# Optimization experiments

Hardware: AMD Instinct MI355X
Metric: run time of the kernel (lower is better)

Reference implementation:

```python
import jax, jax.numpy as jnp
import numpy as np

B, S, D, H, DH, DF = 8, 1024, 512, 8, 64, 2048
EPS = 1e-5


def layer_norm(x, g, b):
    mu = jnp.mean(x, axis=-1, keepdims=True)
    var = jnp.mean(jnp.square(x - mu), axis=-1, keepdims=True)
    return (x - mu) * jax.lax.rsqrt(var + EPS) * g + b


def rel_shift(x):
    # Transformer-XL relative shift: [b,h,q,k] -> shifted [b,h,q,k]
    b, h, q, k = x.shape
    x = jnp.pad(x, ((0, 0), (0, 0), (0, 0), (1, 0)))
    x = x.reshape(b, h, k + 1, q)[:, :, 1:, :].reshape(b, h, q, k)
    return x


def setup_inputs() -> dict:
    key = jax.random.key(0)
    ks = jax.random.split(key, 16)
    sc = 0.02
    inp = {
        'x': jax.random.normal(ks[0], (B, S, D), jnp.float32),
        'rel_positions': jax.random.normal(ks[1], (S, D), jnp.float32),
        'mask': jnp.triu(jnp.ones((S, S), jnp.bool_), k=1),  # True = masked (causal)
        'Wq': jax.random.normal(ks[2], (D, D), jnp.float32) * sc,
        'Wk': jax.random.normal(ks[3], (D, D), jnp.float32) * sc,
        'Wv': jax.random.normal(ks[4], (D, D), jnp.float32) * sc,
        'Wr': jax.random.normal(ks[5], (D, D), jnp.float32) * sc,
        'Wo': jax.random.normal(ks[6], (D, D), jnp.float32) * sc,
        'u_bias': jax.random.normal(ks[7], (H, DH), jnp.float32) * sc,
        'v_bias': jax.random.normal(ks[8], (H, DH), jnp.float32) * sc,
        'ln1_g': jnp.ones((D,), jnp.float32),
        'ln1_b': jnp.zeros((D,), jnp.float32),
        'W1': jax.random.normal(ks[9], (D, DF), jnp.float32) * sc,
        'b1': jnp.zeros((DF,), jnp.float32),
        'W2': jax.random.normal(ks[10], (DF, D), jnp.float32) * sc,
        'b2': jnp.zeros((D,), jnp.float32),
        'ln2_g': jnp.ones((D,), jnp.float32),
        'ln2_b': jnp.zeros((D,), jnp.float32),
    }
    return inp


def reference(x, rel_positions, mask, Wq, Wk, Wv, Wr, Wo, u_bias, v_bias,
              ln1_g, ln1_b, W1, b1, W2, b2, ln2_g, ln2_b):
    b, s, d = x.shape
    q = (x @ Wq).reshape(b, s, H, DH)
    k = (x @ Wk).reshape(b, s, H, DH)
    v = (x @ Wv).reshape(b, s, H, DH)
    r = (rel_positions @ Wr).reshape(s, H, DH)
    # content term (q + u) k^T and position term (q + v) r^T with rel-shift
    ac = jnp.einsum('bqhd,bkhd->bhqk', q + u_bias, k)
    bd = rel_shift(jnp.einsum('bqhd,khd->bhqk', q + v_bias, r))
    scores = (ac + bd) * (1.0 / np.sqrt(DH))
    scores = jnp.where(mask[None, None, :, :], jnp.asarray(-1e9, scores.dtype), scores)
    attn = jax.nn.softmax(scores, axis=-1)
    ctx = jnp.einsum('bhqk,bkhd->bqhd', attn, v).reshape(b, s, d) @ Wo
    h1 = layer_norm(x + ctx, ln1_g, ln1_b)
    ff = jax.nn.relu(h1 @ W1 + b1) @ W2 + b2
    out = layer_norm(h1 + ff, ln2_g, ln2_b)
    return out, attn
```

## Files before the change

### kernel.cpp

```cpp
#include <hip/hip_runtime.h>
#include <hip/hip_bf16.h>

typedef __hip_bfloat16 bf16;

#define NB 8
#define NS 1024
#define ND 512
#define NH 8
#define NDH 64
#define NDF 2048

typedef __attribute__((ext_vector_type(8))) short s16x8;
typedef __attribute__((ext_vector_type(4))) float f32x4;

__device__ __forceinline__ void storev(float* p, float v) { *p = v; }
__device__ __forceinline__ void storev(bf16* p, float v) { *p = __float2bfloat16(v); }
__device__ __forceinline__ short f2bf(float f) {
    bf16 h = __float2bfloat16(f);
    return *reinterpret_cast<short*>(&h);
}
__device__ __forceinline__ float bf2f(short s) {
    bf16 h = *reinterpret_cast<bf16*>(&s);
    return __bfloat162float(h);
}

__device__ __forceinline__ void gload_lds16(const short* g, short* l) {
    __builtin_amdgcn_global_load_lds(
        (const __attribute__((address_space(1))) unsigned int*)g,
        (__attribute__((address_space(3))) unsigned int*)l, 16, 0, 0);
}

__global__ __launch_bounds__(256) void cast2_kernel(
    const float4* __restrict__ inA, int n4a,
    const float4* __restrict__ inB, int n4b,
    short* __restrict__ outA, short* __restrict__ outB)
{
    int i = blockIdx.x * 256 + threadIdx.x;
    const float4* s; short* d; int j;
    if (i < n4a) { s = inA; d = outA; j = i; }
    else if (i < n4a + n4b) { s = inB; d = outB; j = i - n4a; }
    else return;
    float4 v = s[j];
    short4 o;
    o.x = f2bf(v.x); o.y = f2bf(v.y); o.z = f2bf(v.z); o.w = f2bf(v.w);
    *reinterpret_cast<short4*>(d + (size_t)j * 4) = o;
}

struct TP7 {
    const float* src[7];
    short* dst[7];
    int K[7];
    int N[7];
};

__global__ __launch_bounds__(256) void transpose_cast_all_kernel(TP7 p)
{
    __shared__ float t[32][33];
    const int z = blockIdx.z;
    const float* src = p.src[z];
    short* dst = p.dst[z];
    const int K = p.K[z], N = p.N[z];
    const int ntx = N >> 5;
    const int f = blockIdx.x;
    if (f >= ntx * (K >> 5)) return;
    const int n0 = (f % ntx) * 32, k0 = (f / ntx) * 32;
    const int tx = threadIdx.x & 31, ty = threadIdx.x >> 5;
#pragma unroll
    for (int i = 0; i < 4; ++i)
        t[ty + i * 8][tx] = src[(size_t)(k0 + ty + i * 8) * N + n0 + tx];
    __syncthreads();
#pragma unroll
    for (int i = 0; i < 4; ++i)
        dst[(size_t)(n0 + ty + i * 8) * K + k0 + tx] = f2bf(t[tx][ty + i * 8]);
}

__global__ __launch_bounds__(256) void transpose_v_kernel(
    const short* __restrict__ v, short* __restrict__ vT)
{
    __shared__ short t[32][33];
    const int s0 = blockIdx.x * 32, n0 = blockIdx.y * 32;
    const int bh = blockIdx.z;
    const int h = bh & (NH - 1), b = bh >> 3;
    const int tx = threadIdx.x & 31, ty = threadIdx.x >> 5;
#pragma unroll
    for (int i = 0; i < 4; ++i)
        t[ty + i * 8][tx] = v[(size_t)(b * NS + s0 + ty + i * 8) * ND + h * NDH + n0 + tx];
    __syncthreads();
#pragma unroll
    for (int i = 0; i < 4; ++i)
        vT[((size_t)bh * NDH + n0 + ty + i * 8) * NS + s0 + tx] = t[tx][ty + i * 8];
}

template <typename CT>
__global__ __launch_bounds__(256) void mfma_gemm_kernel(
    const short* __restrict__ A, const short* __restrict__ Bt,
    const float* __restrict__ bias, CT* __restrict__ C,
    int M, int N, int K, int doRelu)
{
    __shared__ __align__(16) short As[128 * 32];
    __shared__ __align__(16) short Bs[128 * 32];
    const int row0 = blockIdx.y * 128;
    const int col0 = blockIdx.x * 128;
    const int tid = threadIdx.x;
    const int lane = tid & 63, w = tid >> 6;
    const int wm = w >> 1, wn = w & 1;
    const int lm = lane & 15, kq = lane >> 4;
    const int srow = lane >> 2;
    const int schk = lane & 3;

    f32x4 acc[4][4] = {};

    for (int k0 = 0; k0 < K; k0 += 32) {
#pragma unroll
        for (int p = 0; p < 2; ++p) {
            int rbase = p * 64 + w * 16;
            int r = rbase + srow;
            int gc = schk ^ ((r >> 1) & 3);
            gload_lds16(A  + (size_t)(row0 + r) * K + k0 + gc * 8, As + rbase * 32);
            gload_lds16(Bt + (size_t)(col0 + r) * K + k0 + gc * 8, Bs + rbase * 32);
        }
        __syncthreads();

        s16x8 af[4], bfr[4];
#pragma unroll
        for (int i = 0; i < 4; ++i) {
            int ra = wm * 64 + i * 16 + lm;
            int rb = wn * 64 + i * 16 + lm;
            af[i]  = *reinterpret_cast<const s16x8*>(As + ra * 32 + (kq ^ ((ra >> 1) & 3)) * 8);
            bfr[i] = *reinterpret_cast<const s16x8*>(Bs + rb * 32 + (kq ^ ((rb >> 1) & 3)) * 8);
        }
#pragma unroll
        for (int i = 0; i < 4; ++i)
#pragma unroll
            for (int j = 0; j < 4; ++j)
                acc[i][j] = __builtin_amdgcn_mfma_f32_16x16x32_bf16(
                    af[i], bfr[j], acc[i][j], 0, 0, 0);
        __syncthreads();
    }

#pragma unroll
    for (int i = 0; i < 4; ++i) {
        int cr0 = row0 + wm * 64 + i * 16 + kq * 4;
#pragma unroll
        for (int j = 0; j < 4; ++j) {
            int cc = col0 + wn * 64 + j * 16 + lm;
            float bv = bias ? bias[cc] : 0.0f;
#pragma unroll
            for (int r = 0; r < 4; ++r) {
                float v = acc[i][j][r] + bv;
                if (doRelu) v = fmaxf(v, 0.0f);
                storev(&C[(size_t)(cr0 + r) * N + cc], v);
            }
        }
    }
}

template <typename CT>
__global__ __launch_bounds__(256) void mfma_gemm64_kernel(
    const short* __restrict__ A, const short* __restrict__ Bt,
    const float* __restrict__ bias, CT* __restrict__ C,
    int M, int N, int K, int doRelu)
{
    __shared__ __align__(16) short As[128 * 32];
    __shared__ __align__(16) short Bs[64 * 32];
    const int row0 = blockIdx.y * 128;
    const int col0 = blockIdx.x * 64;
    const int tid = threadIdx.x;
    const int lane = tid & 63, w = tid >> 6;
    const int wm = w >> 1, wn = w & 1;
    const int lm = lane & 15, kq = lane >> 4;
    const int srow = lane >> 2;
    const int schk = lane & 3;

    f32x4 acc[4][2] = {};

    for (int k0 = 0; k0 < K; k0 += 32) {
#pragma unroll
        for (int p = 0; p < 2; ++p) {
            int rbase = p * 64 + w * 16;
            int r = rbase + srow;
            int gc = schk ^ ((r >> 1) & 3);
            gload_lds16(A + (size_t)(row0 + r) * K + k0 + gc * 8, As + rbase * 32);
        }
        {
            int rbase = w * 16;
            int r = rbase + srow;
            int gc = schk ^ ((r >> 1) & 3);
            gload_lds16(Bt + (size_t)(col0 + r) * K + k0 + gc * 8, Bs + rbase * 32);
        }
        __syncthreads();

        s16x8 af[4], bfr[2];
#pragma unroll
        for (int i = 0; i < 4; ++i) {
            int ra = wm * 64 + i * 16 + lm;
            af[i] = *reinterpret_cast<const s16x8*>(As + ra * 32 + (kq ^ ((ra >> 1) & 3)) * 8);
        }
#pragma unroll
        for (int j = 0; j < 2; ++j) {
            int rb = wn * 32 + j * 16 + lm;
            bfr[j] = *reinterpret_cast<const s16x8*>(Bs + rb * 32 + (kq ^ ((rb >> 1) & 3)) * 8);
        }
#pragma unroll
        for (int i = 0; i < 4; ++i)
#pragma unroll
            for (int j = 0; j < 2; ++j)
                acc[i][j] = __builtin_amdgcn_mfma_f32_16x16x32_bf16(
                    af[i], bfr[j], acc[i][j], 0, 0, 0);
        __syncthreads();
    }

#pragma unroll
    for (int i = 0; i < 4; ++i) {
        int cr0 = row0 + wm * 64 + i * 16 + kq * 4;
#pragma unroll
        for (int j = 0; j < 2; ++j) {
            int cc = col0 + wn * 32 + j * 16 + lm;
            float bv = bias ? bias[cc] : 0.0f;
#pragma unroll
            for (int r = 0; r < 4; ++r) {
                float v = acc[i][j][r] + bv;
                if (doRelu) v = fmaxf(v, 0.0f);
                storev(&C[(size_t)(cr0 + r) * N + cc], v);
            }
        }
    }
}

__global__ __launch_bounds__(256) void qkvr_gemm_kernel(
    const short* __restrict__ x_bf, const short* __restrict__ Wqkv,
    const short* __restrict__ rel_bf, const short* __restrict__ WrT,
    const float* __restrict__ ub, const float* __restrict__ vb,
    short* __restrict__ qu, short* __restrict__ qv,
    short* __restrict__ kb, short* __restrict__ vbuf,
    short* __restrict__ r_bf)
{
    const int isRel = blockIdx.x >= 12;
    if (isRel && blockIdx.y >= 8) return;
    const short* A  = isRel ? rel_bf : x_bf;
    const short* Bt = isRel ? WrT : Wqkv;
    const int col0 = isRel ? (blockIdx.x - 12) * 128 : blockIdx.x * 128;
    const int row0 = blockIdx.y * 128;

    __shared__ __align__(16) short As[128 * 32];
    __shared__ __align__(16) short Bs[128 * 32];
    const int tid = threadIdx.x;
    const int lane = tid & 63, w = tid >> 6;
    const int wm = w >> 1, wn = w & 1;
    const int lm = lane & 15, kq = lane >> 4;
    const int srow = lane >> 2;
    const int schk = lane & 3;

    f32x4 acc[4][4] = {};

    for (int k0 = 0; k0 < ND; k0 += 32) {
#pragma unroll
        for (int p = 0; p < 2; ++p) {
            int rbase = p * 64 + w * 16;
            int r = rbase + srow;
            int gc = schk ^ ((r >> 1) & 3);
            gload_lds16(A  + (size_t)(row0 + r) * ND + k0 + gc * 8, As + rbase * 32);
            gload_lds16(Bt + (size_t)(col0 + r) * ND + k0 + gc * 8, Bs + rbase * 32);
        }
        __syncthreads();

        s16x8 af[4], bfr[4];
#pragma unroll
        for (int i = 0; i < 4; ++i) {
            int ra = wm * 64 + i * 16 + lm;
            int rb = wn * 64 + i * 16 + lm;
            af[i]  = *reinterpret_cast<const s16x8*>(As + ra * 32 + (kq ^ ((ra >> 1) & 3)) * 8);
            bfr[i] = *reinterpret_cast<const s16x8*>(Bs + rb * 32 + (kq ^ ((rb >> 1) & 3)) * 8);
        }
#pragma unroll
        for (int i = 0; i < 4; ++i)
#pragma unroll
            for (int j = 0; j < 4; ++j)
                acc[i][j] = __builtin_amdgcn_mfma_f32_16x16x32_bf16(
                    af[i], bfr[j], acc[i][j], 0, 0, 0);
        __syncthreads();
    }

    const int sec = col0 >> 9;
#pragma unroll
    for (int i = 0; i < 4; ++i) {
        int cr0 = row0 + wm * 64 + i * 16 + kq * 4;
#pragma unroll
        for (int j = 0; j < 4; ++j) {
            int cc = col0 + wn * 64 + j * 16 + lm;
            int c5 = cc & 511;
#pragma unroll
            for (int r = 0; r < 4; ++r) {
                float a = acc[i][j][r];
                size_t idx = (size_t)(cr0 + r) * ND + c5;
                if (isRel) {
                    r_bf[idx] = f2bf(a);
                } else if (sec == 0) {
                    qu[idx] = f2bf(a + ub[c5]);
                    qv[idx] = f2bf(a + vb[c5]);
                } else if (sec == 1) {
                    kb[idx] = f2bf(a);
                } else {
                    vbuf[idx] = f2bf(a);
                }
            }
        }
    }
}

__global__ __launch_bounds__(256) void fused_attn_kernel(
    const short* __restrict__ qu, const short* __restrict__ qv,
    const short* __restrict__ kb, const short* __restrict__ rb,
    const short* __restrict__ vT, float* __restrict__ attn,
    short* __restrict__ ctx)
{
    __shared__ __align__(16) short K_s[64 * 64];
    __shared__ __align__(16) short V_s[64 * 64];
    __shared__ __align__(16) short r_s[2][64 * 64];
    __shared__ __align__(16) short bd_s[64][80];

    const int bid = blockIdx.x;
    const int strip = 15 - (bid >> 6);
    const int bh = bid & 63;
    const int h = bh & (NH - 1), b = bh >> 3;
    const int q0 = strip * 64;
    const int n_kt = strip + 1;
    const int tid = threadIdx.x;
    const int lane = tid & 63, w = tid >> 6;
    const int lm = lane & 15, kq = lane >> 4;
    const int woff = 48 - w * 16;
    const int srow8 = lane >> 3;
    const int schk8 = lane & 7;

    s16x8 aq[2], av[2];
#pragma unroll
    for (int ks = 0; ks < 2; ++ks) {
        const size_t off = (size_t)(b * NS + q0 + w * 16 + lm) * ND + h * NDH + ks * 32 + kq * 8;
        aq[ks] = *reinterpret_cast<const s16x8*>(qu + off);
        av[ks] = *reinterpret_cast<const s16x8*>(qv + off);
    }

    f32x4 apv[4] = {};
    float linv[4];

    for (int pass = 0; pass < 2; ++pass) {
        float lsum[4] = {0.f, 0.f, 0.f, 0.f};
        for (int kt = 0; kt < n_kt; ++kt) {
            const int k0 = kt * 64;
            const int ub0 = k0 - q0 + 960;
            __syncthreads();
#pragma unroll
            for (int p = 0; p < 2; ++p) {
                int rbase = p * 32 + w * 8;
                int grow = rbase + srow8;
                int gc = schk8 ^ (grow & 7);
                gload_lds16(kb + (size_t)(b * NS + k0 + grow) * ND + h * NDH + gc * 8,
                            K_s + rbase * 64);
            }
            if (pass) {
#pragma unroll
                for (int p = 0; p < 2; ++p) {
                    int rbase = p * 32 + w * 8;
                    int grow = rbase + srow8;
                    int gc = schk8 ^ (grow & 7);
                    gload_lds16(vT + ((size_t)bh * NDH + grow) * NS + k0 + gc * 8,
                                V_s + rbase * 64);
                }
            }
            if (kt == 0) {
#pragma unroll
                for (int half = 0; half < 2; ++half)
#pragma unroll
                    for (int p = 0; p < 2; ++p) {
                        int rbase = p * 32 + w * 8;
                        int grow = rbase + srow8;
                        int ur = ub0 + half * 64 + grow; ur = ur > 1023 ? 1023 : ur;
                        int gc = schk8 ^ (grow & 7);
                        gload_lds16(rb + (size_t)ur * ND + h * NDH + gc * 8,
                                    r_s[half] + rbase * 64);
                    }
            } else {
#pragma unroll
                for (int p = 0; p < 2; ++p) {
                    int rbase = p * 32 + w * 8;
                    int grow = rbase + srow8;
                    int ur = ub0 + 64 + grow; ur = ur > 1023 ? 1023 : ur;
                    int gc = schk8 ^ (grow & 7);
                    gload_lds16(rb + (size_t)ur * ND + h * NDH + gc * 8,
                                r_s[(kt + 1) & 1] + rbase * 64);
                }
            }
            __syncthreads();

            f32x4 aac[4] = {};
            f32x4 abd[5] = {};
            __builtin_amdgcn_s_setprio(1);
#pragma unroll
            for (int ks = 0; ks < 2; ++ks) {
#pragma unroll
                for (int j = 0; j < 4; ++j) {
                    int rr = j * 16 + lm;
                    s16x8 bk = *reinterpret_cast<const s16x8*>(
                        K_s + rr * 64 + ((4 * ks + kq) ^ (lm & 7)) * 8);
                    aac[j] = __builtin_amdgcn_mfma_f32_16x16x32_bf16(aq[ks], bk, aac[j], 0, 0, 0);
                }
#pragma unroll
                for (int j = 0; j < 5; ++j) {
                    int rr = woff + j * 16 + lm;
                    const short* rbuf = r_s[(kt + (rr >> 6)) & 1];
                    s16x8 br = *reinterpret_cast<const s16x8*>(
                        rbuf + (rr & 63) * 64 + ((4 * ks + kq) ^ (lm & 7)) * 8);
                    abd[j] = __builtin_amdgcn_mfma_f32_16x16x32_bf16(av[ks], br, abd[j], 0, 0, 0);
                }
            }
            __builtin_amdgcn_s_setprio(0);
#pragma unroll
            for (int j = 0; j < 5; ++j)
#pragma unroll
                for (int r = 0; r < 4; ++r)
                    bd_s[w * 16 + kq * 4 + r][j * 16 + lm] = f2bf(abd[j][r]);

            float sv[4][4];
#pragma unroll
            for (int jj = 0; jj < 4; ++jj)
#pragma unroll
                for (int r = 0; r < 4; ++r) {
                    int c = jj * 16 + lm - kq * 4 - r + 15;
                    sv[jj][r] = (aac[jj][r] + bf2f(bd_s[w * 16 + kq * 4 + r][c])) * 0.125f;
                }

            if (pass == 0) {
#pragma unroll
                for (int jj = 0; jj < 4; ++jj)
#pragma unroll
                    for (int r = 0; r < 4; ++r) {
                        int q_ls = w * 16 + kq * 4 + r;
                        bool ok = (k0 + jj * 16 + lm) <= (q0 + q_ls);
                        lsum[r] += ok ? __expf(sv[jj][r]) : 0.0f;
                    }
            } else {
                short* ew = &bd_s[w * 16][0];
#pragma unroll
                for (int jj = 0; jj < 4; ++jj)
#pragma unroll
                    for (int r = 0; r < 4; ++r) {
                        int q_ls = w * 16 + kq * 4 + r;
                        int kk = k0 + jj * 16 + lm;
                        bool ok = kk <= (q0 + q_ls);
                        float a = ok ? __expf(sv[jj][r]) * linv[r] : 0.0f;
                        attn[((size_t)bh * NS + q0 + q_ls) * NS + kk] = a;
                        ew[(kq * 4 + r) * 80 + jj * 16 + lm] = f2bf(a);
                    }
#pragma unroll
                for (int ks = 0; ks < 2; ++ks) {
                    s16x8 ae = *reinterpret_cast<const s16x8*>(ew + lm * 80 + ks * 32 + kq * 8);
#pragma unroll
                    for (int jn = 0; jn < 4; ++jn) {
                        s16x8 bv = *reinterpret_cast<const s16x8*>(
                            V_s + (jn * 16 + lm) * 64 + ((4 * ks + kq) ^ (lm & 7)) * 8);
                        apv[jn] = __builtin_amdgcn_mfma_f32_16x16x32_bf16(ae, bv, apv[jn], 0, 0, 0);
                    }
                }
            }
        }
        if (pass == 0) {
#pragma unroll
            for (int r = 0; r < 4; ++r) {
                float v = lsum[r];
                v += __shfl_xor(v, 1); v += __shfl_xor(v, 2);
                v += __shfl_xor(v, 4); v += __shfl_xor(v, 8);
                linv[r] = 1.0f / v;
            }
        }
    }

    const int z = NS - n_kt * 64;
    if (z > 0) {
        const int z4 = z >> 2;
        float4 zz = make_float4(0.f, 0.f, 0.f, 0.f);
        for (int i = tid; i < 64 * z4; i += 256) {
            int zr = i / z4, zc = i - zr * z4;
            *reinterpret_cast<float4*>(
                attn + ((size_t)bh * NS + q0 + zr) * NS + n_kt * 64 + zc * 4) = zz;
        }
    }
#pragma unroll
    for (int jn = 0; jn < 4; ++jn)
#pragma unroll
        for (int r = 0; r < 4; ++r)
            ctx[(size_t)(b * NS + q0 + w * 16 + kq * 4 + r) * ND + h * NDH + jn * 16 + lm] =
                f2bf(apv[jn][r]);
}

__global__ __launch_bounds__(256) void add_ln_kernel(
    const float* __restrict__ xin, const float* __restrict__ yin,
    const float* __restrict__ g, const float* __restrict__ bb,
    float* __restrict__ out, short* __restrict__ out_bf)
{
    __shared__ float red[4];
    __shared__ float red2[4];
    const int row = blockIdx.x;
    const size_t base = (size_t)row * ND;
    const int tid = threadIdx.x;
    const int lane = tid & 63, w = tid >> 6;

    float v0 = xin[base + tid] + yin[base + tid];
    float v1 = xin[base + tid + 256] + yin[base + tid + 256];
    float s = v0 + v1;
#pragma unroll
    for (int o = 32; o > 0; o >>= 1) s += __shfl_xor(s, o);
    if (lane == 0) red[w] = s;
    __syncthreads();
    float mu = (red[0] + red[1] + red[2] + red[3]) * (1.0f / ND);
    float d0 = v0 - mu, d1 = v1 - mu;
    float vs = d0 * d0 + d1 * d1;
#pragma unroll
    for (int o = 32; o > 0; o >>= 1) vs += __shfl_xor(vs, o);
    if (lane == 0) red2[w] = vs;
    __syncthreads();
    float var = (red2[0] + red2[1] + red2[2] + red2[3]) * (1.0f / ND);
    float rs = rsqrtf(var + 1e-5f);
    float o0 = d0 * rs * g[tid] + bb[tid];
    float o1 = d1 * rs * g[tid + 256] + bb[tid + 256];
    out[base + tid] = o0;
    out[base + tid + 256] = o1;
    if (out_bf) {
        out_bf[base + tid] = f2bf(o0);
        out_bf[base + tid + 256] = f2bf(o1);
    }
}

extern "C" void kernel_launch(void* const* d_in, const int* in_sizes, int n_in,
                              void* d_out, int out_size, void* d_ws, size_t ws_size,
                              hipStream_t stream)
{
    const float* x   = (const float*)d_in[0];
    const float* rel = (const float*)d_in[1];
    const float* Wq = (const float*)d_in[3];
    const float* Wk = (const float*)d_in[4];
    const float* Wv = (const float*)d_in[5];
    const float* Wr = (const float*)d_in[6];
    const float* Wo = (const float*)d_in[7];
    const float* ub = (const float*)d_in[8];
    const float* vb = (const float*)d_in[9];
    const float* g1 = (const float*)d_in[10];
    const float* be1 = (const float*)d_in[11];
    const float* W1 = (const float*)d_in[12];
    const float* bb1 = (const float*)d_in[13];
    const float* W2 = (const float*)d_in[14];
    const float* bb2 = (const float*)d_in[15];
    const float* g2 = (const float*)d_in[16];
    const float* be2 = (const float*)d_in[17];

    float* out0 = (float*)d_out;
    float* attn = out0 + (size_t)NB * NS * ND;

    char* ws = (char*)d_ws;
    const size_t SZ_F32 = (size_t)NB * NS * ND * 4;
    const size_t SZ_BF  = (size_t)NB * NS * ND * 2;
    const size_t SZ_MID = (size_t)NB * NS * NDF * 2;
    const size_t SZ_RBF = (size_t)NS * ND * 2;
    const size_t SZ_W   = (size_t)ND * ND * 2;
    const size_t SZ_W12 = (size_t)ND * NDF * 2;
    const size_t needed = 2 * SZ_F32 + 8 * SZ_BF + SZ_MID + 2 * SZ_RBF + 5 * SZ_W + 2 * SZ_W12;
    if (ws_size < needed) return;

    float* tmp  = (float*)ws; ws += SZ_F32;
    float* h1   = (float*)ws; ws += SZ_F32;
    short* x_bf = (short*)ws; ws += SZ_BF;
    short* qu_bf = (short*)ws; ws += SZ_BF;
    short* qv_bf = (short*)ws; ws += SZ_BF;
    short* k_bf = (short*)ws; ws += SZ_BF;
    short* vbuf = (short*)ws; ws += SZ_BF;
    short* vT   = (short*)ws; ws += SZ_BF;
    short* ctx  = (short*)ws; ws += SZ_BF;
    short* h1b  = (short*)ws; ws += SZ_BF;
    short* mid  = (short*)ws; ws += SZ_MID;
    short* rel_bf = (short*)ws; ws += SZ_RBF;
    short* r_bf   = (short*)ws; ws += SZ_RBF;
    short* Wqkv = (short*)ws; ws += 3 * SZ_W;
    short* WrT = (short*)ws; ws += SZ_W;
    short* WoT = (short*)ws; ws += SZ_W;
    short* W1T = (short*)ws; ws += SZ_W12;
    short* W2T = (short*)ws; ws += SZ_W12;

    dim3 blk(256);
    const int M = NB * NS;

    cast2_kernel<<<dim3((M * ND / 4 + NS * ND / 4 + 255) / 256), blk, 0, stream>>>(
        (const float4*)x, M * ND / 4, (const float4*)rel, NS * ND / 4, x_bf, rel_bf);
    TP7 tp;
    tp.src[0] = Wq; tp.dst[0] = Wqkv;                 tp.K[0] = ND;  tp.N[0] = ND;
    tp.src[1] = Wk; tp.dst[1] = Wqkv + (size_t)ND * ND;     tp.K[1] = ND;  tp.N[1] = ND;
    tp.src[2] = Wv; tp.dst[2] = Wqkv + (size_t)2 * ND * ND; tp.K[2] = ND;  tp.N[2] = ND;
    tp.src[3] = Wr; tp.dst[3] = WrT;                  tp.K[3] = ND;  tp.N[3] = ND;
    tp.src[4] = Wo; tp.dst[4] = WoT;                  tp.K[4] = ND;  tp.N[4] = ND;
    tp.src[5] = W1; tp.dst[5] = W1T;                  tp.K[5] = ND;  tp.N[5] = NDF;
    tp.src[6] = W2; tp.dst[6] = W2T;                  tp.K[6] = NDF; tp.N[6] = ND;
    transpose_cast_all_kernel<<<dim3(1024, 1, 7), blk, 0, stream>>>(tp);

    qkvr_gemm_kernel<<<dim3(16, M / 128), blk, 0, stream>>>(
        x_bf, Wqkv, rel_bf, WrT, ub, vb, qu_bf, qv_bf, k_bf, vbuf, r_bf);
    transpose_v_kernel<<<dim3(NS / 32, NDH / 32, NB * NH), blk, 0, stream>>>(vbuf, vT);

    fused_attn_kernel<<<dim3(NB * NH * 16), blk, 0, stream>>>(
        qu_bf, qv_bf, k_bf, r_bf, vT, attn, ctx);

    mfma_gemm64_kernel<float><<<dim3(ND / 64, M / 128), blk, 0, stream>>>(
        ctx, WoT, nullptr, tmp, M, ND, ND, 0);
    add_ln_kernel<<<dim3(M), blk, 0, stream>>>(x, tmp, g1, be1, h1, h1b);

    mfma_gemm_kernel<bf16><<<dim3(NDF / 128, M / 128), blk, 0, stream>>>(
        h1b, W1T, bb1, (bf16*)mid, M, NDF, ND, 1);
    mfma_gemm64_kernel<float><<<dim3(ND / 64, M / 128), blk, 0, stream>>>(
        mid, W2T, bb2, tmp, M, ND, NDF, 0);
    add_ln_kernel<<<dim3(M), blk, 0, stream>>>(h1, tmp, g2, be2, out0, nullptr);
}
```

Baseline: 299.5 us.

## Enlarge attention query tile to 128 rows with 512-thread blocks

```diff
diff --git a/kernel.cpp b/kernel.cpp
--- a/kernel.cpp
+++ b/kernel.cpp
@@ -308,7 +308,7 @@
     }
 }
 
-__global__ __launch_bounds__(256) void fused_attn_kernel(
+__global__ __launch_bounds__(512, 4) void fused_attn_kernel(
     const short* __restrict__ qu, const short* __restrict__ qv,
     const short* __restrict__ kb, const short* __restrict__ rb,
     const short* __restrict__ vT, float* __restrict__ attn,
@@ -316,19 +316,20 @@
 {
     __shared__ __align__(16) short K_s[64 * 64];
     __shared__ __align__(16) short V_s[64 * 64];
-    __shared__ __align__(16) short r_s[2][64 * 64];
-    __shared__ __align__(16) short bd_s[64][80];
+    __shared__ __align__(16) short r_s[3][64 * 64];
+    __shared__ __align__(16) short bd_s[128][80];
 
     const int bid = blockIdx.x;
-    const int strip = 15 - (bid >> 6);
+    const int sidx = bid >> 6;
+    const int st = (sidx < 4) ? (7 - sidx) : (sidx - 4);
     const int bh = bid & 63;
     const int h = bh & (NH - 1), b = bh >> 3;
-    const int q0 = strip * 64;
-    const int n_kt = strip + 1;
+    const int q0 = st * 128;
+    const int n_kt = 2 * st + 2;
     const int tid = threadIdx.x;
     const int lane = tid & 63, w = tid >> 6;
     const int lm = lane & 15, kq = lane >> 4;
-    const int woff = 48 - w * 16;
+    const int woff = 112 - w * 16;
     const int srow8 = lane >> 3;
     const int schk8 = lane & 7;
 
@@ -347,47 +348,35 @@
         float lsum[4] = {0.f, 0.f, 0.f, 0.f};
         for (int kt = 0; kt < n_kt; ++kt) {
             const int k0 = kt * 64;
-            const int ub0 = k0 - q0 + 960;
+            const int bk0 = kt - 2 * st + 14;
             __syncthreads();
-#pragma unroll
-            for (int p = 0; p < 2; ++p) {
-                int rbase = p * 32 + w * 8;
+            {
+                int rbase = w * 8;
                 int grow = rbase + srow8;
                 int gc = schk8 ^ (grow & 7);
                 gload_lds16(kb + (size_t)(b * NS + k0 + grow) * ND + h * NDH + gc * 8,
                             K_s + rbase * 64);
             }
             if (pass) {
-#pragma unroll
-                for (int p = 0; p < 2; ++p) {
-                    int rbase = p * 32 + w * 8;
+                int rbase = w * 8;
+                int grow = rbase + srow8;
+                int gc = schk8 ^ (grow & 7);
+                gload_lds16(vT + ((size_t)bh * NDH + grow) * NS + k0 + gc * 8,
+                            V_s + rbase * 64);
+            }
+            {
+                int i0 = (kt == 0) ? 0 : 2;
+#pragma unroll
+                for (int i = 0; i < 3; ++i) {
+                    if (i < i0) continue;
+                    int blk = bk0 + i;
+                    int slot = blk % 3;
+                    int rbase = w * 8;
                     int grow = rbase + srow8;
-                    int gc = schk8 ^ (grow & 7);
-                    gload_lds16(vT + ((size_t)bh * NDH + grow) * NS + k0 + gc * 8,
-                                V_s + rbase * 64);
-                }
-            }
-            if (kt == 0) {
-#pragma unroll
-                for (int half = 0; half < 2; ++half)
-#pragma unroll
-                    for (int p = 0; p < 2; ++p) {
-                        int rbase = p * 32 + w * 8;
-                        int grow = rbase + srow8;
-                        int ur = ub0 + half * 64 + grow; ur = ur > 1023 ? 1023 : ur;
-                        int gc = schk8 ^ (grow & 7);
-                        gload_lds16(rb + (size_t)ur * ND + h * NDH + gc * 8,
-                                    r_s[half] + rbase * 64);
-                    }
-            } else {
-#pragma unroll
-                for (int p = 0; p < 2; ++p) {
-                    int rbase = p * 32 + w * 8;
-                    int grow = rbase + srow8;
-                    int ur = ub0 + 64 + grow; ur = ur > 1023 ? 1023 : ur;
+                    int ur = blk * 64 + grow; ur = ur > 1023 ? 1023 : ur;
                     int gc = schk8 ^ (grow & 7);
                     gload_lds16(rb + (size_t)ur * ND + h * NDH + gc * 8,
-                                r_s[(kt + 1) & 1] + rbase * 64);
+                                r_s[slot] + rbase * 64);
                 }
             }
             __syncthreads();
@@ -407,9 +396,9 @@
 #pragma unroll
                 for (int j = 0; j < 5; ++j) {
                     int rr = woff + j * 16 + lm;
-                    const short* rbuf = r_s[(kt + (rr >> 6)) & 1];
+                    int slot = (bk0 + (rr >> 6)) % 3;
                     s16x8 br = *reinterpret_cast<const s16x8*>(
-                        rbuf + (rr & 63) * 64 + ((4 * ks + kq) ^ (lm & 7)) * 8);
+                        r_s[slot] + (rr & 63) * 64 + ((4 * ks + kq) ^ (lm & 7)) * 8);
                     abd[j] = __builtin_amdgcn_mfma_f32_16x16x32_bf16(av[ks], br, abd[j], 0, 0, 0);
                 }
             }
@@ -420,25 +409,26 @@
                 for (int r = 0; r < 4; ++r)
                     bd_s[w * 16 + kq * 4 + r][j * 16 + lm] = f2bf(abd[j][r]);
 
-            float sv[4][4];
-#pragma unroll
-            for (int jj = 0; jj < 4; ++jj)
-#pragma unroll
-                for (int r = 0; r < 4; ++r) {
-                    int c = jj * 16 + lm - kq * 4 - r + 15;
-                    sv[jj][r] = (aac[jj][r] + bf2f(bd_s[w * 16 + kq * 4 + r][c])) * 0.125f;
-                }
-
             if (pass == 0) {
 #pragma unroll
                 for (int jj = 0; jj < 4; ++jj)
 #pragma unroll
                     for (int r = 0; r < 4; ++r) {
                         int q_ls = w * 16 + kq * 4 + r;
+                        int c = jj * 16 + lm - kq * 4 - r + 15;
+                        float s = (aac[jj][r] + bf2f(bd_s[q_ls][c])) * 0.125f;
                         bool ok = (k0 + jj * 16 + lm) <= (q0 + q_ls);
-                        lsum[r] += ok ? __expf(sv[jj][r]) : 0.0f;
+                        lsum[r] += ok ? __expf(s) : 0.0f;
                     }
             } else {
+                float sv[4][4];
+#pragma unroll
+                for (int jj = 0; jj < 4; ++jj)
+#pragma unroll
+                    for (int r = 0; r < 4; ++r) {
+                        int c = jj * 16 + lm - kq * 4 - r + 15;
+                        sv[jj][r] = (aac[jj][r] + bf2f(bd_s[w * 16 + kq * 4 + r][c])) * 0.125f;
+                    }
                 short* ew = &bd_s[w * 16][0];
 #pragma unroll
                 for (int jj = 0; jj < 4; ++jj)
@@ -478,7 +468,7 @@
     if (z > 0) {
         const int z4 = z >> 2;
         float4 zz = make_float4(0.f, 0.f, 0.f, 0.f);
-        for (int i = tid; i < 64 * z4; i += 256) {
+        for (int i = tid; i < 128 * z4; i += 512) {
             int zr = i / z4, zc = i - zr * z4;
             *reinterpret_cast<float4*>(
                 attn + ((size_t)bh * NS + q0 + zr) * NS + n_kt * 64 + zc * 4) = zz;
@@ -603,7 +593,7 @@
         x_bf, Wqkv, rel_bf, WrT, ub, vb, qu_bf, qv_bf, k_bf, vbuf, r_bf);
     transpose_v_kernel<<<dim3(NS / 32, NDH / 32, NB * NH), blk, 0, stream>>>(vbuf, vT);
 
-    fused_attn_kernel<<<dim3(NB * NH * 16), blk, 0, stream>>>(
+    fused_attn_kernel<<<dim3(NB * NH * 8), dim3(512), 0, stream>>>(
         qu_bf, qv_bf, k_bf, r_bf, vT, attn, ctx);
 
     mfma_gemm64_kernel<float><<<dim3(ND / 64, M / 128), blk, 0, stream>>>(
```

After: 350.6 us. 17.1% more time.
